# Kernel tuning notes

Measured on AMD Instinct MI355X. Metric: run time of the kernel, lower is better.

## Reference

```python
import jax, jax.numpy as jnp
import numpy as np

E = 384      # hidden_dim
H = 8        # num_attention_heads
D = E // H   # head_dim = 48


def setup_inputs() -> dict:
    key = jax.random.key(0)
    ks = jax.random.split(key, 11)
    B, S = 4, 2048
    patch_embeds = jax.random.normal(ks[0], (B, S, E), dtype=jnp.float32)
    attention_mask = jax.random.randint(ks[1], (B, S), 0, 2).astype(bool)
    s = 1.0 / np.sqrt(E)
    Wq = jax.random.normal(ks[2], (E, E), dtype=jnp.float32) * s
    bq = jnp.zeros((E,), dtype=jnp.float32)
    Wk = jax.random.normal(ks[3], (E, E), dtype=jnp.float32) * s
    bk = jnp.zeros((E,), dtype=jnp.float32)
    Wv = jax.random.normal(ks[4], (E, E), dtype=jnp.float32) * s
    bv = jnp.zeros((E,), dtype=jnp.float32)
    Wo = jax.random.normal(ks[5], (E, E), dtype=jnp.float32) * s
    bo = jnp.zeros((E,), dtype=jnp.float32)
    return {"patch_embeds": patch_embeds, "attention_mask": attention_mask,
            "Wq": Wq, "bq": bq, "Wk": Wk, "bk": bk,
            "Wv": Wv, "bv": bv, "Wo": Wo, "bo": bo}


def reference(patch_embeds, attention_mask, Wq, bq, Wk, bk, Wv, bv, Wo, bo):
    B, S, _ = patch_embeds.shape
    scale = D ** (-0.5)
    # QKV projections (nn.Linear: x @ W.T + b); W stored as [out,in]
    q = patch_embeds @ Wq.T + bq
    k = patch_embeds @ Wk.T + bk
    v = patch_embeds @ Wv.T + bv
    # [B,S,E] -> [B,H,S,D]
    q = q.reshape(B, S, H, D).transpose(0, 2, 1, 3)
    k = k.reshape(B, S, H, D).transpose(0, 2, 1, 3)
    v = v.reshape(B, S, H, D).transpose(0, 2, 1, 3)
    # scaled dot-product attention with key mask (True = masked)
    scores = jnp.einsum('bhqd,bhkd->bhqk', q, k) * scale
    mask = attention_mask[:, None, None, :]  # [B,1,1,S]
    scores = jnp.where(mask, -jnp.inf, scores)
    weights = jax.nn.softmax(scores, axis=-1)
    out = jnp.einsum('bhqk,bhkd->bhqd', weights, v)
    out = out.transpose(0, 2, 1, 3).reshape(B, S, E)
    return out @ Wo.T + bo
```

## Files before the change

### kernel.cpp

```cpp
#include <hip/hip_runtime.h>
#include <math.h>

#define B_ 4
#define S_ 2048
#define E_ 384
#define H_ 8
#define D_ 48
#define M_ (B_*S_)
#define DP_ 64
constexpr float QK_SCALE = 0.14433756729740643f * 1.4426950408889634f;

typedef __attribute__((ext_vector_type(8))) short short8;
typedef __attribute__((ext_vector_type(4))) float f32x4;
typedef __attribute__((ext_vector_type(4))) unsigned uint4v;
typedef unsigned short u16;

__device__ inline u16 f2bf(float f) {
    unsigned u = __float_as_uint(f);
    return (u16)((u + 0x7FFFu + ((u >> 16) & 1u)) >> 16);
}
__device__ inline float bf2f(u16 h) { return __uint_as_float(((unsigned)h) << 16); }
__device__ inline unsigned pk2(float a, float b) {
    return (unsigned)f2bf(a) | ((unsigned)f2bf(b) << 16);
}
__device__ inline unsigned pk2_fast(float a, float b) {
#if __has_builtin(__builtin_amdgcn_perm)
    unsigned ua = __float_as_uint(a) + 0x8000u;
    unsigned ub = __float_as_uint(b) + 0x8000u;
    return __builtin_amdgcn_perm(ub, ua, 0x07060302u);
#else
    return pk2(a, b);
#endif
}
__device__ inline float fexp2(float x) {
#if __has_builtin(__builtin_amdgcn_exp2f)
    return __builtin_amdgcn_exp2f(x);
#else
    return exp2f(x);
#endif
}
__device__ inline void glld16(const void* g, void* l) {
    __builtin_amdgcn_global_load_lds((const __attribute__((address_space(1))) unsigned int*)g,
                                     (__attribute__((address_space(3))) unsigned int*)l, 16, 0, 0);
}
__device__ inline void plswap32(unsigned &a, unsigned &b) {
#if __has_builtin(__builtin_amdgcn_permlane32_swap)
    auto r = __builtin_amdgcn_permlane32_swap(a, b, false, false);
    a = r[0]; b = r[1];
#else
    asm volatile("v_permlane32_swap_b32 %0, %1" : "+v"(a), "+v"(b));
#endif
}
__device__ inline void plswap16(unsigned &a, unsigned &b) {
#if __has_builtin(__builtin_amdgcn_permlane16_swap)
    auto r = __builtin_amdgcn_permlane16_swap(a, b, false, false);
    a = r[0]; b = r[1];
#else
    asm volatile("v_permlane16_swap_b32 %0, %1" : "+v"(a), "+v"(b));
#endif
}

__global__ __launch_bounds__(256) void prep(const float4* __restrict__ x,
                                            const int* __restrict__ mask,
                                            const float4* __restrict__ wq,
                                            const float4* __restrict__ wk,
                                            const float4* __restrict__ wv,
                                            const float4* __restrict__ wo,
                                            uint2* __restrict__ xb,
                                            uint2* __restrict__ wb,
                                            u16* __restrict__ Qp, u16* __restrict__ Kp) {
    const int bx = blockIdx.x, t = threadIdx.x;
    if (bx < 3072) {
        int i = bx * 256 + t;
        float4 v = x[i];
        uint2 H;
        H.x = pk2(v.x, v.y);
        H.y = pk2(v.z, v.w);
        xb[i] = H;
    } else if (bx < 3072 + 144) {
        int i = (bx - 3072) * 256 + t;
        const int n4 = 36864;
        const float4* srcs[4] = {wq, wk, wv, wo};
        #pragma unroll
        for (int j = 0; j < 4; ++j) {
            float4 v = srcs[j][i];
            uint2 H;
            H.x = pk2(v.x, v.y);
            H.y = pk2(v.z, v.w);
            wb[(size_t)j * n4 + i] = H;
        }
    } else {
        int i = (bx - 3216) * 256 + t;
        int bh = i >> 11, s = i & 2047, b = bh >> 3;
        size_t off = ((size_t)bh * S_ + s) * DP_ + 48;
        uint4 qz = {0x00004300u, 0, 0, 0};
        uint4 kz = {mask[b * S_ + s] ? 0x0000BF80u : 0u, 0, 0, 0};
        uint4 z  = {0, 0, 0, 0};
        *reinterpret_cast<uint4*>(Qp + off)     = qz;
        *reinterpret_cast<uint4*>(Qp + off + 8) = z;
        *reinterpret_cast<uint4*>(Kp + off)     = kz;
        *reinterpret_cast<uint4*>(Kp + off + 8) = z;
    }
}

__global__ __launch_bounds__(256) void gemm_qkv3(const u16* __restrict__ xb,
                                                 const u16* __restrict__ wb,
                                                 const float* __restrict__ bq,
                                                 const float* __restrict__ bk,
                                                 const float* __restrict__ bv,
                                                 u16* __restrict__ Qp, u16* __restrict__ Kp,
                                                 u16* __restrict__ Vtp) {
    __shared__ u16 smem[4 * 4096];
    u16* As = smem;

    const int t = threadIdx.x, w = t >> 6, lane = t & 63;
    const int ln = lane & 15, quad = lane >> 4;
    const int gr = lane >> 3;
    const int gc = (lane & 7) ^ gr;
    const int m0 = blockIdx.x * 64;
    const int n0 = blockIdx.y * 64;
    const int b  = m0 >> 11;

    const u16* aSrc = xb + (size_t)(m0 + w * 16 + gr) * E_ + gc * 8;
    const u16* wSrc0 = wb + (size_t)0 * 147456 + (size_t)(n0 + w * 16 + gr) * E_ + gc * 8;
    const u16* wSrc1 = wb + (size_t)1 * 147456 + (size_t)(n0 + w * 16 + gr) * E_ + gc * 8;
    const u16* wSrc2 = wb + (size_t)2 * 147456 + (size_t)(n0 + w * 16 + gr) * E_ + gc * 8;

    f32x4 acc[3][4];
    #pragma unroll
    for (int j = 0; j < 3; ++j)
        #pragma unroll
        for (int nt = 0; nt < 4; ++nt)
            acc[j][nt] = (f32x4){0.f, 0.f, 0.f, 0.f};

    short8 rA0, rA1, rW[3][2];
    auto loads = [&](int kk) {
        rA0 = *reinterpret_cast<const short8*>(aSrc + kk);
        rA1 = *reinterpret_cast<const short8*>(aSrc + 8 * E_ + kk);
        #pragma unroll
        for (int i = 0; i < 2; ++i) {
            rW[0][i] = *reinterpret_cast<const short8*>(wSrc0 + i * 8 * E_ + kk);
            rW[1][i] = *reinterpret_cast<const short8*>(wSrc1 + i * 8 * E_ + kk);
            rW[2][i] = *reinterpret_cast<const short8*>(wSrc2 + i * 8 * E_ + kk);
        }
    };
    auto writes = [&]() {
        *reinterpret_cast<short8*>(As + (w * 16) * 64 + lane * 8)     = rA0;
        *reinterpret_cast<short8*>(As + (w * 16 + 8) * 64 + lane * 8) = rA1;
        #pragma unroll
        for (int j = 0; j < 3; ++j)
            #pragma unroll
            for (int i = 0; i < 2; ++i)
                *reinterpret_cast<short8*>(smem + (1 + j) * 4096 +
                                           (w * 16 + i * 8) * 64 + lane * 8) = rW[j][i];
    };

    loads(0);
    writes();
    __syncthreads();

    #pragma unroll
    for (int it = 0; it < 6; ++it) {
        if (it < 5) loads((it + 1) * 64);

        #pragma unroll
        for (int ks = 0; ks < 2; ++ks) {
            const int slot = (ks * 4 + quad) ^ (ln & 7);
            short8 ah = *reinterpret_cast<const short8*>(&As[(w * 16 + ln) * 64 + slot * 8]);
            #pragma unroll
            for (int j = 0; j < 3; ++j) {
                const u16* Wsj = smem + (1 + j) * 4096;
                #pragma unroll
                for (int nt = 0; nt < 4; ++nt) {
                    short8 wf = *reinterpret_cast<const short8*>(&Wsj[(nt * 16 + ln) * 64 + slot * 8]);
                    acc[j][nt] = __builtin_amdgcn_mfma_f32_16x16x32_bf16(ah, wf, acc[j][nt], 0, 0, 0);
                }
            }
        }
        __syncthreads();
        if (it < 5) {
            writes();
            __syncthreads();
        }
    }

    {
        const int s_base = (m0 & 2047) + w * 16 + quad * 4;
        #pragma unroll
        for (int nt = 0; nt < 4; ++nt) {
            const int col = n0 + nt * 16 + ln;
            const int h   = (col * 683) >> 15;
            const int d   = col - h * 48;
            const float bc = bv[col];
            u16* dst = Vtp + ((size_t)(b * 8 + h) * 48 + d) * 2048;
            uint2 pk;
            pk.x = pk2(acc[2][nt][0] + bc, acc[2][nt][1] + bc);
            pk.y = pk2(acc[2][nt][2] + bc, acc[2][nt][3] + bc);
            *reinterpret_cast<uint2*>(dst + s_base) = pk;
        }
    }

    u16* TrQ = smem;
    u16* TrK = smem + 64 * 76;
    __syncthreads();
    #pragma unroll
    for (int nt = 0; nt < 4; ++nt) {
        const int col = n0 + nt * 16 + ln;
        const float bcq = bq[col], bck = bk[col];
        #pragma unroll
        for (int r = 0; r < 4; ++r) {
            int row = w * 16 + quad * 4 + r;
            TrQ[row * 76 + nt * 16 + ln] = f2bf((acc[0][nt][r] + bcq) * QK_SCALE);
            TrK[row * 76 + nt * 16 + ln] = f2bf(acc[1][nt][r] + bck);
        }
    }
    __syncthreads();
    {
        const int row = t >> 2, quarter = t & 3;
        const int s   = (m0 & 2047) + row;
        #pragma unroll
        for (int c = 0; c < 2; ++c) {
            int gcol = n0 + quarter * 16 + c * 8;
            int h = (gcol * 683) >> 15;
            int d = gcol - h * 48;
            size_t off = ((size_t)(b * 8 + h) * 2048 + s) * DP_ + d;
            *reinterpret_cast<uint4*>(Qp + off) =
                *reinterpret_cast<const uint4*>(&TrQ[row * 76 + quarter * 16 + c * 8]);
            *reinterpret_cast<uint4*>(Kp + off) =
                *reinterpret_cast<const uint4*>(&TrK[row * 76 + quarter * 16 + c * 8]);
        }
    }
}

__global__ __launch_bounds__(256) void gemm_out(const u16* __restrict__ ab,
                                                const u16* __restrict__ wb,
                                                const float* __restrict__ bo, float* __restrict__ out) {
    __shared__ u16 smem[2 * 4096 + 2 * 4096];
    u16* As = smem;
    u16* Ws = smem + 2 * 4096;
    const int t = threadIdx.x, w = t >> 6, lane = t & 63;
    const int ln = lane & 15, quad = lane >> 4;
    const int gr = lane >> 3;
    const int gc = (lane & 7) ^ gr;
    const int m0 = blockIdx.x * 64, n0 = blockIdx.y * 64;
    const u16* wh = wb + (size_t)3 * 147456;

    f32x4 acc[4];
    #pragma unroll
    for (int nt = 0; nt < 4; ++nt) acc[nt] = (f32x4){0.f, 0.f, 0.f, 0.f};

    auto stage = [&](int bf, int kk) {
        #pragma unroll
        for (int i = 0; i < 2; ++i) {
            int r0 = w * 16 + i * 8;
            glld16(ab + (size_t)(m0 + r0 + gr) * E_ + kk + gc * 8, As + bf * 4096 + r0 * 64);
            glld16(wh + (size_t)(n0 + r0 + gr) * E_ + kk + gc * 8, Ws + bf * 4096 + r0 * 64);
        }
    };

    stage(0, 0);
    __syncthreads();
    #pragma unroll
    for (int it = 0; it < 6; ++it) {
        const int cur = it & 1;
        if (it < 5) stage(cur ^ 1, (it + 1) * 64);
        const u16* Ab = As + cur * 4096;
        const u16* Wb = Ws + cur * 4096;
        #pragma unroll
        for (int ks = 0; ks < 2; ++ks) {
            const int slot = (ks * 4 + quad) ^ (ln & 7);
            short8 ah = *reinterpret_cast<const short8*>(&Ab[(w * 16 + ln) * 64 + slot * 8]);
            #pragma unroll
            for (int nt = 0; nt < 4; ++nt) {
                short8 wf = *reinterpret_cast<const short8*>(&Wb[(nt * 16 + ln) * 64 + slot * 8]);
                acc[nt] = __builtin_amdgcn_mfma_f32_16x16x32_bf16(ah, wf, acc[nt], 0, 0, 0);
            }
        }
        __syncthreads();
    }

    #pragma unroll
    for (int nt = 0; nt < 4; ++nt) {
        const int col = n0 + nt * 16 + ln;
        const float bc = bo[col];
        #pragma unroll
        for (int r = 0; r < 4; ++r) {
            size_t row = (size_t)(m0 + w * 16 + quad * 4 + r);
            out[row * E_ + col] = acc[nt][r] + bc;
        }
    }
}

__global__ __launch_bounds__(512, 4) void attn_mfma(const u16* __restrict__ Qp,
                                                    const u16* __restrict__ Kp,
                                                    const u16* __restrict__ Vtp,
                                                    u16* __restrict__ AO) {
    __shared__ __align__(16) u16 QPs[128 * 64];
    __shared__ __align__(16) u16 Ksh[2][128 * 64];
    __shared__ __align__(16) u16 Vt[2][2][48 * 64];
    __shared__ float linv[8][16];

    const int t    = threadIdx.x;
    const int w    = t >> 6;
    const int lane = t & 63;
    const int ln   = lane & 15;
    const int quad = lane >> 4;
    const int gr   = lane >> 3;
    const int gc   = (lane & 7) ^ gr;
    const int bh   = blockIdx.x;
    const int q0   = blockIdx.y * 128;
    const int b    = bh >> 3, h = bh & 7;
    const int cb   = h * 48;
    const size_t rb = (size_t)b * S_;

    const u16* Qsrc = Qp  + ((size_t)bh * S_ + q0) * DP_;
    const u16* Ksrc = Kp  + (size_t)bh * S_ * DP_;
    const u16* Vsrc = Vtp + (size_t)bh * 48 * 2048;

    const int swz0 = ((quad    ) ^ (ln & 7)) << 3;
    const int swz1 = ((4 + quad) ^ (ln & 7)) << 3;
    const u16* kA[2][2];
    const u16* vA[2][4];
    #pragma unroll
    for (int bf = 0; bf < 2; ++bf) {
        kA[bf][0] = &Ksh[bf][ln * 64 + swz0];
        kA[bf][1] = &Ksh[bf][ln * 64 + swz1];
        #pragma unroll
        for (int g = 0; g < 4; ++g)
            vA[bf][g] = &Vt[bf][g >> 1][ln * 64 + ((((g & 1) * 4 + quad) ^ (ln & 7)) << 3)];
    }
    const int qrow = (w * 16 + ln) * 64;
    const u16* pR[2];
    pR[0] = &QPs[qrow + swz0];
    pR[1] = &QPs[qrow + swz1];

    auto stage = [&](int bf, int kt) {
        const int k0 = kt * 128;
        #pragma unroll
        for (int i = 0; i < 2; ++i)
            glld16(Ksrc + (size_t)(k0 + w * 16 + i * 8 + gr) * DP_ + gc * 8,
                   &Ksh[bf][(w * 16 + i * 8) * 64]);
        if (w < 6) {
            glld16(Vsrc + (size_t)(w * 8 + gr) * 2048 + k0 + gc * 8,      &Vt[bf][0][(w * 8) * 64]);
            glld16(Vsrc + (size_t)(w * 8 + gr) * 2048 + k0 + 64 + gc * 8, &Vt[bf][1][(w * 8) * 64]);
        }
    };

    #pragma unroll
    for (int i = 0; i < 2; ++i) {
        int r0 = w * 16 + i * 8;
        glld16(Qsrc + (size_t)(r0 + gr) * DP_ + gc * 8, &QPs[r0 * 64]);
    }
    stage(0, 0);
    __syncthreads();

    short8 qf[2];
    qf[0] = *reinterpret_cast<const short8*>(pR[0]);
    qf[1] = *reinterpret_cast<const short8*>(pR[1]);

    f32x4 o[3];
    #pragma unroll
    for (int nt = 0; nt < 3; ++nt) o[nt] = (f32x4){0.f, 0.f, 0.f, 0.f};
    float lq = 0.f;

    auto body = [&](int cur, int nxt, int ktn) {
        if (ktn < 16) stage(nxt, ktn);

        short8 pa[4];
        #pragma unroll
        for (int hf = 0; hf < 2; ++hf) {
            f32x4 sc[4];
            #pragma unroll
            for (int m = 0; m < 4; ++m) {
                const int Mt = hf * 4 + m;
                short8 kf0 = *reinterpret_cast<const short8*>(kA[cur][0] + Mt * 1024);
                short8 kf1 = *reinterpret_cast<const short8*>(kA[cur][1] + Mt * 1024);
                f32x4 a0 = __builtin_amdgcn_mfma_f32_16x16x32_bf16(kf0, qf[0], (f32x4){0.f,0.f,0.f,0.f}, 0, 0, 0);
                sc[m] = __builtin_amdgcn_mfma_f32_16x16x32_bf16(kf1, qf[1], a0, 0, 0, 0);
            }
            unsigned U[4][2];
            #pragma unroll
            for (int m = 0; m < 4; ++m) {
                float p0 = fexp2(sc[m][0]);
                float p1 = fexp2(sc[m][1]);
                float p2 = fexp2(sc[m][2]);
                float p3 = fexp2(sc[m][3]);
                lq += (p0 + p1) + (p2 + p3);
                U[m][0] = pk2_fast(p0, p1);
                U[m][1] = pk2_fast(p2, p3);
            }
            #pragma unroll
            for (int g = 0; g < 2; ++g) {
                unsigned a0 = U[g * 2][0], b0 = U[g * 2 + 1][0];
                plswap32(a0, b0); plswap16(a0, b0);
                unsigned a1 = U[g * 2][1], b1 = U[g * 2 + 1][1];
                plswap32(a1, b1); plswap16(a1, b1);
                uint4v uv = {a0, a1, b0, b1};
                pa[hf * 2 + g] = __builtin_bit_cast(short8, uv);
            }
        }

        #pragma unroll
        for (int nt = 0; nt < 3; ++nt)
            #pragma unroll
            for (int g = 0; g < 4; ++g) {
                short8 vb = *reinterpret_cast<const short8*>(vA[cur][g] + nt * 1024);
                o[nt] = __builtin_amdgcn_mfma_f32_16x16x32_bf16(pa[g], vb, o[nt], 0, 0, 0);
            }
        __syncthreads();
    };

    for (int kt = 0; kt < 16; kt += 2) {
        body(0, 1, kt + 1);
        body(1, 0, kt + 2);
    }

    {
        float l = lq;
        l += __shfl_xor(l, 16);
        l += __shfl_xor(l, 32);
        if (quad == 0) linv[w][ln] = 1.0f / l;
    }
    __syncthreads();
    {
        f32x4 il = *reinterpret_cast<const f32x4*>(&linv[w][quad * 4]);
        #pragma unroll
        for (int nt = 0; nt < 3; ++nt)
            #pragma unroll
            for (int r = 0; r < 4; ++r) {
                size_t row = rb + q0 + w * 16 + quad * 4 + r;
                size_t idx = row * E_ + cb + nt * 16 + ln;
                AO[idx] = f2bf(o[nt][r] * il[r]);
            }
    }
}

extern "C" void kernel_launch(void* const* d_in, const int* in_sizes, int n_in,
                              void* d_out, int out_size, void* d_ws, size_t ws_size,
                              hipStream_t stream) {
    (void)in_sizes; (void)n_in; (void)out_size; (void)ws_size;
    const float* x    = (const float*)d_in[0];
    const int*   mask = (const int*)  d_in[1];
    const float* Wq   = (const float*)d_in[2];
    const float* bq   = (const float*)d_in[3];
    const float* Wk   = (const float*)d_in[4];
    const float* bk   = (const float*)d_in[5];
    const float* Wv   = (const float*)d_in[6];
    const float* bv   = (const float*)d_in[7];
    const float* Wo   = (const float*)d_in[8];
    const float* bo   = (const float*)d_in[9];

    const size_t NELEM = (size_t)M_ * E_;
    const size_t WELEM = (size_t)E_ * E_;
    const size_t PEL   = (size_t)B_ * H_ * S_ * DP_;
    u16* ws = (u16*)d_ws;
    u16* xb  = ws;
    u16* wb  = xb + NELEM;
    u16* Qp  = wb + 4 * WELEM;
    u16* Kp  = Qp + PEL;
    u16* Vtp = Kp + PEL;
    u16* AO  = xb;

    dim3 blk(256);
    prep<<<dim3(3472), blk, 0, stream>>>(
        (const float4*)x, mask,
        (const float4*)Wq, (const float4*)Wk, (const float4*)Wv, (const float4*)Wo,
        (uint2*)xb, (uint2*)wb, Qp, Kp);

    gemm_qkv3<<<dim3(M_ / 64, 6), blk, 0, stream>>>(xb, wb, bq, bk, bv, Qp, Kp, Vtp);

    attn_mfma<<<dim3(B_ * H_, S_ / 128), dim3(512), 0, stream>>>(Qp, Kp, Vtp, AO);

    gemm_out<<<dim3(M_ / 64, 6), blk, 0, stream>>>(AO, wb, bo, (float*)d_out);
}
```

Before: 146.7 us.

## Triple-buffer K tiles and prefetch two tiles ahead with partial vmcnt waits

Replaces the K/V double buffer with a three-slot K pool and a two-slot V pool, with the Q staging buffer reused as the third K slot. K is now prefetched two iterations ahead and V one ahead. The end-of-iteration __syncthreads is replaced by a partial s_waitcnt vmcnt plus s_barrier, so outstanding loads can stay in flight across the barrier. V's shared layout is also reorganised into a single 128-wide swizzled tile. The aim is to hide global load latency better, at the cost of more complex hand-managed waitcnt accounting and an extra barrier after Q is read.

```diff
diff --git a/kernel.cpp b/kernel.cpp
--- a/kernel.cpp
+++ b/kernel.cpp
@@ -295,9 +295,8 @@
                                                     const u16* __restrict__ Kp,
                                                     const u16* __restrict__ Vtp,
                                                     u16* __restrict__ AO) {
-    __shared__ __align__(16) u16 QPs[128 * 64];
-    __shared__ __align__(16) u16 Ksh[2][128 * 64];
-    __shared__ __align__(16) u16 Vt[2][2][48 * 64];
+    __shared__ __align__(16) u16 kpool[3][128 * 64];
+    __shared__ __align__(16) u16 vpool[2][48 * 128];
     __shared__ float linv[8][16];
 
     const int t    = threadIdx.x;
@@ -307,6 +306,8 @@
     const int quad = lane >> 4;
     const int gr   = lane >> 3;
     const int gc   = (lane & 7) ^ gr;
+    const int vr   = lane >> 4;
+    const int vc   = lane & 15;
     const int bh   = blockIdx.x;
     const int q0   = blockIdx.y * 128;
     const int b    = bh >> 3, h = bh & 7;
@@ -319,52 +320,62 @@
 
     const int swz0 = ((quad    ) ^ (ln & 7)) << 3;
     const int swz1 = ((4 + quad) ^ (ln & 7)) << 3;
-    const u16* kA[2][2];
+    const u16* kA[3][2];
     const u16* vA[2][4];
     #pragma unroll
-    for (int bf = 0; bf < 2; ++bf) {
-        kA[bf][0] = &Ksh[bf][ln * 64 + swz0];
-        kA[bf][1] = &Ksh[bf][ln * 64 + swz1];
+    for (int bf = 0; bf < 3; ++bf) {
+        kA[bf][0] = &kpool[bf][ln * 64 + swz0];
+        kA[bf][1] = &kpool[bf][ln * 64 + swz1];
+    }
+    #pragma unroll
+    for (int bf = 0; bf < 2; ++bf)
         #pragma unroll
         for (int g = 0; g < 4; ++g)
-            vA[bf][g] = &Vt[bf][g >> 1][ln * 64 + ((((g & 1) * 4 + quad) ^ (ln & 7)) << 3)];
-    }
+            vA[bf][g] = &vpool[bf][ln * 128 + (((g * 4 + quad) ^ (ln & 7)) << 3)];
     const int qrow = (w * 16 + ln) * 64;
-    const u16* pR[2];
-    pR[0] = &QPs[qrow + swz0];
-    pR[1] = &QPs[qrow + swz1];
-
-    auto stage = [&](int bf, int kt) {
+
+    auto stageK = [&](u16* dst, int kt) {
         const int k0 = kt * 128;
         #pragma unroll
         for (int i = 0; i < 2; ++i)
             glld16(Ksrc + (size_t)(k0 + w * 16 + i * 8 + gr) * DP_ + gc * 8,
-                   &Ksh[bf][(w * 16 + i * 8) * 64]);
+                   dst + (w * 16 + i * 8) * 64);
+    };
+    auto stageV = [&](u16* dst, int kt) {
         if (w < 6) {
-            glld16(Vsrc + (size_t)(w * 8 + gr) * 2048 + k0 + gc * 8,      &Vt[bf][0][(w * 8) * 64]);
-            glld16(Vsrc + (size_t)(w * 8 + gr) * 2048 + k0 + 64 + gc * 8, &Vt[bf][1][(w * 8) * 64]);
+            const int k0 = kt * 128;
+            #pragma unroll
+            for (int j = 0; j < 2; ++j) {
+                const int vrow = w * 8 + j * 4 + vr;
+                glld16(Vsrc + (size_t)vrow * 2048 + k0 + (vc ^ (vrow & 7)) * 8,
+                       dst + (w * 8 + j * 4) * 128);
+            }
         }
     };
 
     #pragma unroll
     for (int i = 0; i < 2; ++i) {
         int r0 = w * 16 + i * 8;
-        glld16(Qsrc + (size_t)(r0 + gr) * DP_ + gc * 8, &QPs[r0 * 64]);
-    }
-    stage(0, 0);
+        glld16(Qsrc + (size_t)(r0 + gr) * DP_ + gc * 8, &kpool[2][r0 * 64]);
+    }
+    stageV(vpool[0], 0);
+    stageK(kpool[0], 0);
+    stageK(kpool[1], 1);
     __syncthreads();
 
     short8 qf[2];
-    qf[0] = *reinterpret_cast<const short8*>(pR[0]);
-    qf[1] = *reinterpret_cast<const short8*>(pR[1]);
+    qf[0] = *reinterpret_cast<const short8*>(&kpool[2][qrow + swz0]);
+    qf[1] = *reinterpret_cast<const short8*>(&kpool[2][qrow + swz1]);
+    __syncthreads();
 
     f32x4 o[3];
     #pragma unroll
     for (int nt = 0; nt < 3; ++nt) o[nt] = (f32x4){0.f, 0.f, 0.f, 0.f};
     float lq = 0.f;
 
-    auto body = [&](int cur, int nxt, int ktn) {
-        if (ktn < 16) stage(nxt, ktn);
+    auto body = [&](int kb, int kbN2, int vb, int ktn, int stmode, int wmode) {
+        if (stmode >= 1) stageV(vpool[vb ^ 1], ktn + 1);
+        if (stmode == 2) stageK(kpool[kbN2], ktn + 2);
 
         short8 pa[4];
         #pragma unroll
@@ -373,8 +384,8 @@
             #pragma unroll
             for (int m = 0; m < 4; ++m) {
                 const int Mt = hf * 4 + m;
-                short8 kf0 = *reinterpret_cast<const short8*>(kA[cur][0] + Mt * 1024);
-                short8 kf1 = *reinterpret_cast<const short8*>(kA[cur][1] + Mt * 1024);
+                short8 kf0 = *reinterpret_cast<const short8*>(kA[kb][0] + Mt * 1024);
+                short8 kf1 = *reinterpret_cast<const short8*>(kA[kb][1] + Mt * 1024);
                 f32x4 a0 = __builtin_amdgcn_mfma_f32_16x16x32_bf16(kf0, qf[0], (f32x4){0.f,0.f,0.f,0.f}, 0, 0, 0);
                 sc[m] = __builtin_amdgcn_mfma_f32_16x16x32_bf16(kf1, qf[1], a0, 0, 0, 0);
             }
@@ -404,16 +415,33 @@
         for (int nt = 0; nt < 3; ++nt)
             #pragma unroll
             for (int g = 0; g < 4; ++g) {
-                short8 vb = *reinterpret_cast<const short8*>(vA[cur][g] + nt * 1024);
-                o[nt] = __builtin_amdgcn_mfma_f32_16x16x32_bf16(pa[g], vb, o[nt], 0, 0, 0);
-            }
-        __syncthreads();
+                short8 vb8 = *reinterpret_cast<const short8*>(vA[vb][g] + nt * 2048);
+                o[nt] = __builtin_amdgcn_mfma_f32_16x16x32_bf16(pa[g], vb8, o[nt], 0, 0, 0);
+            }
+
+        if (wmode == 0) {
+            asm volatile("s_waitcnt vmcnt(2)" ::: "memory");
+            __builtin_amdgcn_s_barrier();
+        } else if (wmode == 1) {
+            asm volatile("s_waitcnt vmcnt(0)" ::: "memory");
+            __builtin_amdgcn_s_barrier();
+        }
     };
 
-    for (int kt = 0; kt < 16; kt += 2) {
-        body(0, 1, kt + 1);
-        body(1, 0, kt + 2);
-    }
+    #pragma unroll 1
+    for (int rep = 0; rep < 2; ++rep) {
+        const int t6 = rep * 6;
+        body(0, 2, 0, t6 + 0, 2, 0);
+        body(1, 0, 1, t6 + 1, 2, 0);
+        body(2, 1, 0, t6 + 2, 2, 0);
+        body(0, 2, 1, t6 + 3, 2, 0);
+        body(1, 0, 0, t6 + 4, 2, 0);
+        body(2, 1, 1, t6 + 5, 2, 0);
+    }
+    body(0, 2, 0, 12, 2, 0);
+    body(1, 0, 1, 13, 2, 0);
+    body(2, 1, 0, 14, 1, 1);
+    body(0, 2, 1, 15, 0, 2);
 
     {
         float l = lq;
```

Measured after the change: 197.2 us. 34.4% more time.
